# Kernel optimization log

Hardware: AMD Instinct MI355X
Metric: run time of the kernel (lower is better)

The kernel has to match this reference:

```python
import jax, jax.numpy as jnp
import numpy as np

N_NODES = 100000
N_EDGES = 1600000
D_FEAT = 64
EPS = 1e-07


def setup_inputs() -> dict:
    key = jax.random.key(0)
    k1, k2, k3 = jax.random.split(key, 3)
    x = jax.random.normal(k1, (N_NODES, D_FEAT), dtype=jnp.float32)
    beta = jnp.ones((1,), dtype=jnp.float32)
    edge_row = jnp.sort(jax.random.randint(k2, (N_EDGES,), 0, N_NODES, dtype=jnp.int64))
    edge_col = jax.random.randint(k3, (N_EDGES,), 0, N_NODES, dtype=jnp.int64)
    return {"x": x, "beta": beta, "edge_row": edge_row, "edge_col": edge_col}


def reference(x, beta, edge_row, edge_col):
    # Gather endpoint features: [E, d]
    A = x[edge_row]
    B = x[edge_col]
    # Cosine similarity per edge, scaled by beta: [E]
    inner = jnp.sum(A * B, axis=1)
    norms = jnp.linalg.norm(A, axis=1) * jnp.linalg.norm(B, axis=1)
    sim = beta[0] * (inner / (norms + EPS))
    # Sparse row-wise softmax (tf.sparse.softmax): stable segment softmax over edges grouped by row
    row_max = jax.ops.segment_max(sim, edge_row, num_segments=N_NODES)
    e = jnp.exp(sim - row_max[edge_row])
    row_sum = jax.ops.segment_sum(e, edge_row, num_segments=N_NODES)
    p = e / row_sum[edge_row]  # [E]
    # SPMM: out[i] = sum_{(i,j) in E} p_ij * x[j]
    out = jax.ops.segment_sum(p[:, None] * B, edge_row, num_segments=N_NODES)
    return out
```

## Files before the change

kernel.cpp:

```cpp
#include <hip/hip_runtime.h>
#include <math.h>

#define D_FEAT 64
typedef _Float16 v8h __attribute__((ext_vector_type(8)));
typedef _Float16 v4h __attribute__((ext_vector_type(4)));
typedef float v4f __attribute__((ext_vector_type(4)));

static __device__ __forceinline__ v8h u2h8(uint4 u){ v8h v; __builtin_memcpy(&v,&u,16); return v; }
static __device__ __forceinline__ v4h u2h4(uint2 u){ v4h v; __builtin_memcpy(&v,&u,8); return v; }
static __device__ __forceinline__ float f16lo(unsigned int m){
    unsigned short us = (unsigned short)(m & 0xffffu);
    _Float16 h; __builtin_memcpy(&h, &us, 2); return (float)h;
}

__global__ __launch_bounds__(256)
void agnn_prep1(const float* __restrict__ x, float* __restrict__ nf,
                uint2* __restrict__ xh, int n_nodes) {
    int t = blockIdx.x*blockDim.x + threadIdx.x;
    int node = t >> 4; if (node >= n_nodes) return;
    int l4 = t & 15;
    float4 v = ((const float4*)x)[node*16 + l4];
    float ss = v.x*v.x + v.y*v.y + v.z*v.z + v.w*v.w;
    #pragma unroll
    for (int off = 1; off < 16; off <<= 1) ss += __shfl_xor(ss, off, 64);
    float r = ss > 0.f ? rsqrtf(ss) : 0.f;
    if (l4 == 0) nf[node] = ss * r;
    auto h0 = __builtin_amdgcn_cvt_pkrtz(v.x*r, v.y*r);
    auto h1 = __builtin_amdgcn_cvt_pkrtz(v.z*r, v.w*r);
    uint2 u; __builtin_memcpy(&u.x, &h0, 4); __builtin_memcpy(&u.y, &h1, 4);
    xh[node*16 + l4] = u;
}

__global__ __launch_bounds__(256)
void agnn_prep2(const int* __restrict__ edge_row, const int* __restrict__ edge_col,
                const float* __restrict__ nf, int* __restrict__ row_ptr,
                unsigned int* __restrict__ md, int n_nodes, int n_edges) {
    int e = blockIdx.x*blockDim.x + threadIdx.x;
    if (e < 64) md[n_edges + e] = 0xFFFF0000u;
    if (e >= n_edges) return;
    int r1 = edge_row[e];
    int r0 = (e == 0) ? -1 : edge_row[e-1];
    for (int r = r0+1; r <= r1; ++r) row_ptr[r] = e;
    if (e == n_edges-1)
        for (int r = r1+1; r <= n_nodes; ++r) row_ptr[r] = n_edges;
    _Float16 h = (_Float16)nf[edge_col[e]];
    unsigned short us; __builtin_memcpy(&us, &h, 2);
    md[e] = ((unsigned int)(r1 & 15) << 16) | us;
}

#define XCP_PITCH 144
__global__ __launch_bounds__(128, 6)
void agnn_fused(const float* __restrict__ beta_p,
                const int* __restrict__ edge_col,
                const unsigned int* __restrict__ md,
                const int* __restrict__ row_ptr,
                const uint4* __restrict__ xh4,
                float* __restrict__ out, int n_nodes) {
    __shared__ char lds_raw[2 * 32 * XCP_PITCH];
    int wid = threadIdx.x >> 6, lane = threadIdx.x & 63;
    int q = lane >> 4, lo4 = lane & 15;
    char* XCP = lds_raw + wid * 32 * XCP_PITCH;

    int t0 = (blockIdx.x*2 + wid) * 16;
    if (t0 >= n_nodes) return;

    int qn = t0 + lo4; if (qn >= n_nodes) qn = n_nodes - 1;
    v8h b0 = u2h8(xh4[(size_t)qn*8 + q]);
    v8h b1 = u2h8(xh4[(size_t)qn*8 + 4 + q]);
    float beta  = beta_p[0];
    float shift = fabsf(beta);
    int te = t0 + 16; if (te > n_nodes) te = n_nodes;
    int es = row_ptr[t0];
    int L  = row_ptr[te] - es;

    v4f o0={0,0,0,0}, o1={0,0,0,0}, o2={0,0,0,0}, o3={0,0,0,0};
    float s = 0.f;
    unsigned int selp = (lo4 & 1) ? 0x07060302u : 0x05040100u;

    for (int base = 0; base < L; base += 32) {
        int i0 = base + lo4;
        int e0 = es + (i0 < L ? i0 : 0);
        int i1 = base + 16 + lo4;
        int e1 = es + (i1 < L ? i1 : 0);
        int c0 = edge_col[e0];
        int c1 = edge_col[e1];
        uint4 A00 = xh4[(size_t)c0*8 + q];
        uint4 A01 = xh4[(size_t)c0*8 + 4 + q];
        uint4 A10 = xh4[(size_t)c1*8 + q];
        uint4 A11 = xh4[(size_t)c1*8 + 4 + q];
        int mb = es + base + 4*q;
        unsigned int m00 = md[mb+0],  m01 = md[mb+1],  m02 = md[mb+2],  m03 = md[mb+3];
        unsigned int m10 = md[mb+16], m11 = md[mb+17], m12 = md[mb+18], m13 = md[mb+19];

        v4f z0 = {0,0,0,0};
        z0 = __builtin_amdgcn_mfma_f32_16x16x32_f16(u2h8(A00), b0, z0, 0,0,0);
        z0 = __builtin_amdgcn_mfma_f32_16x16x32_f16(u2h8(A01), b1, z0, 0,0,0);
        v4f z1 = {0,0,0,0};
        z1 = __builtin_amdgcn_mfma_f32_16x16x32_f16(u2h8(A10), b0, z1, 0,0,0);
        z1 = __builtin_amdgcn_mfma_f32_16x16x32_f16(u2h8(A11), b1, z1, 0,0,0);

        {
            unsigned int colA = lo4*4, colB = (16+lo4)*4;
            char* pA = XCP + (4*q)*XCP_PITCH;
            char* pB = XCP + (16+4*q)*XCP_PITCH;
            *(unsigned int*)(pA + 0*XCP_PITCH + colA) = A00.x;
            *(unsigned int*)(pA + 1*XCP_PITCH + colA) = A00.y;
            *(unsigned int*)(pA + 2*XCP_PITCH + colA) = A00.z;
            *(unsigned int*)(pA + 3*XCP_PITCH + colA) = A00.w;
            *(unsigned int*)(pB + 0*XCP_PITCH + colA) = A01.x;
            *(unsigned int*)(pB + 1*XCP_PITCH + colA) = A01.y;
            *(unsigned int*)(pB + 2*XCP_PITCH + colA) = A01.z;
            *(unsigned int*)(pB + 3*XCP_PITCH + colA) = A01.w;
            *(unsigned int*)(pA + 0*XCP_PITCH + colB) = A10.x;
            *(unsigned int*)(pA + 1*XCP_PITCH + colB) = A10.y;
            *(unsigned int*)(pA + 2*XCP_PITCH + colB) = A10.z;
            *(unsigned int*)(pA + 3*XCP_PITCH + colB) = A10.w;
            *(unsigned int*)(pB + 0*XCP_PITCH + colB) = A11.x;
            *(unsigned int*)(pB + 1*XCP_PITCH + colB) = A11.y;
            *(unsigned int*)(pB + 2*XCP_PITCH + colB) = A11.z;
            *(unsigned int*)(pB + 3*XCP_PITCH + colB) = A11.w;
        }

        int lim0 = L - base - 4*q;
        int lim1 = lim0 - 16;
        float w00 = (0 < lim0 && (m00>>16)==(unsigned)lo4) ? __expf(fmaf(beta, z0[0], -shift)) : 0.f;
        float w01 = (1 < lim0 && (m01>>16)==(unsigned)lo4) ? __expf(fmaf(beta, z0[1], -shift)) : 0.f;
        float w02 = (2 < lim0 && (m02>>16)==(unsigned)lo4) ? __expf(fmaf(beta, z0[2], -shift)) : 0.f;
        float w03 = (3 < lim0 && (m03>>16)==(unsigned)lo4) ? __expf(fmaf(beta, z0[3], -shift)) : 0.f;
        float w10 = (0 < lim1 && (m10>>16)==(unsigned)lo4) ? __expf(fmaf(beta, z1[0], -shift)) : 0.f;
        float w11 = (1 < lim1 && (m11>>16)==(unsigned)lo4) ? __expf(fmaf(beta, z1[1], -shift)) : 0.f;
        float w12 = (2 < lim1 && (m12>>16)==(unsigned)lo4) ? __expf(fmaf(beta, z1[2], -shift)) : 0.f;
        float w13 = (3 < lim1 && (m13>>16)==(unsigned)lo4) ? __expf(fmaf(beta, z1[3], -shift)) : 0.f;
        s += (w00+w01) + (w02+w03) + (w10+w11) + (w12+w13);

        v4h pa0, pa1;
        {
            auto a = __builtin_amdgcn_cvt_pkrtz(w00*f16lo(m00), w01*f16lo(m01));
            auto b = __builtin_amdgcn_cvt_pkrtz(w02*f16lo(m02), w03*f16lo(m03));
            pa0[0]=a[0]; pa0[1]=a[1]; pa0[2]=b[0]; pa0[3]=b[1];
            auto c = __builtin_amdgcn_cvt_pkrtz(w10*f16lo(m10), w11*f16lo(m11));
            auto d = __builtin_amdgcn_cvt_pkrtz(w12*f16lo(m12), w13*f16lo(m13));
            pa1[0]=c[0]; pa1[1]=c[1]; pa1[2]=d[0]; pa1[3]=d[1];
        }

        const char* rbase_p = XCP + (lo4>>1)*XCP_PITCH + 16*q;
        {
            const char* rp = rbase_p;
            uint4 d0 = *(const uint4*)rp;
            uint4 d1 = *(const uint4*)(rp + 64);
            uint2 bb0 = { __builtin_amdgcn_perm(d0.y, d0.x, selp), __builtin_amdgcn_perm(d0.w, d0.z, selp) };
            uint2 bb1 = { __builtin_amdgcn_perm(d1.y, d1.x, selp), __builtin_amdgcn_perm(d1.w, d1.z, selp) };
            o0 = __builtin_amdgcn_mfma_f32_16x16x16f16(pa0, u2h4(bb0), o0, 0,0,0);
            o0 = __builtin_amdgcn_mfma_f32_16x16x16f16(pa1, u2h4(bb1), o0, 0,0,0);
        }
        {
            const char* rp = rbase_p + 8*XCP_PITCH;
            uint4 d0 = *(const uint4*)rp;
            uint4 d1 = *(const uint4*)(rp + 64);
            uint2 bb0 = { __builtin_amdgcn_perm(d0.y, d0.x, selp), __builtin_amdgcn_perm(d0.w, d0.z, selp) };
            uint2 bb1 = { __builtin_amdgcn_perm(d1.y, d1.x, selp), __builtin_amdgcn_perm(d1.w, d1.z, selp) };
            o1 = __builtin_amdgcn_mfma_f32_16x16x16f16(pa0, u2h4(bb0), o1, 0,0,0);
            o1 = __builtin_amdgcn_mfma_f32_16x16x16f16(pa1, u2h4(bb1), o1, 0,0,0);
        }
        {
            const char* rp = rbase_p + 16*XCP_PITCH;
            uint4 d0 = *(const uint4*)rp;
            uint4 d1 = *(const uint4*)(rp + 64);
            uint2 bb0 = { __builtin_amdgcn_perm(d0.y, d0.x, selp), __builtin_amdgcn_perm(d0.w, d0.z, selp) };
            uint2 bb1 = { __builtin_amdgcn_perm(d1.y, d1.x, selp), __builtin_amdgcn_perm(d1.w, d1.z, selp) };
            o2 = __builtin_amdgcn_mfma_f32_16x16x16f16(pa0, u2h4(bb0), o2, 0,0,0);
            o2 = __builtin_amdgcn_mfma_f32_16x16x16f16(pa1, u2h4(bb1), o2, 0,0,0);
        }
        {
            const char* rp = rbase_p + 24*XCP_PITCH;
            uint4 d0 = *(const uint4*)rp;
            uint4 d1 = *(const uint4*)(rp + 64);
            uint2 bb0 = { __builtin_amdgcn_perm(d0.y, d0.x, selp), __builtin_amdgcn_perm(d0.w, d0.z, selp) };
            uint2 bb1 = { __builtin_amdgcn_perm(d1.y, d1.x, selp), __builtin_amdgcn_perm(d1.w, d1.z, selp) };
            o3 = __builtin_amdgcn_mfma_f32_16x16x16f16(pa0, u2h4(bb0), o3, 0,0,0);
            o3 = __builtin_amdgcn_mfma_f32_16x16x16f16(pa1, u2h4(bb1), o3, 0,0,0);
        }
    }

    s += __shfl_xor(s, 16, 64);
    s += __shfl_xor(s, 32, 64);

    #pragma unroll
    for (int r = 0; r < 4; ++r) {
        float sr = __shfl(s, 4*q + r, 64);
        float inv = sr > 0.f ? 1.f/sr : 0.f;
        int node = t0 + 4*q + r;
        if (node < n_nodes) {
            float* p = out + (size_t)node*64 + lo4;
            p[0]  = o0[r]*inv;
            p[16] = o1[r]*inv;
            p[32] = o2[r]*inv;
            p[48] = o3[r]*inv;
        }
    }
}

extern "C" void kernel_launch(void* const* d_in, const int* in_sizes, int n_in,
                              void* d_out, int out_size, void* d_ws, size_t ws_size,
                              hipStream_t stream) {
    const float* x        = (const float*)d_in[0];
    const float* beta     = (const float*)d_in[1];
    const int*   edge_row = (const int*)d_in[2];
    const int*   edge_col = (const int*)d_in[3];
    float* out = (float*)d_out;

    int n_nodes = in_sizes[0] / D_FEAT;
    int n_edges = in_sizes[2];

    char* ws = (char*)d_ws;
    float* nf = (float*)ws;
    size_t off0 = ((size_t)n_nodes*sizeof(float) + 255) & ~(size_t)255;
    int* row_ptr = (int*)(ws + off0);
    size_t off1 = off0 + (((size_t)(n_nodes+1)*sizeof(int) + 255) & ~(size_t)255);
    unsigned int* md = (unsigned int*)(ws + off1);
    size_t off2 = off1 + (((size_t)(n_edges+64)*sizeof(unsigned int) + 255) & ~(size_t)255);
    uint2* xh = (uint2*)(ws + off2);

    {
        long long threads = (long long)n_nodes * 16;
        int blocks = (int)((threads + 255) / 256);
        agnn_prep1<<<blocks, 256, 0, stream>>>(x, nf, xh, n_nodes);
    }
    {
        int blocks = (n_edges + 255) / 256;
        agnn_prep2<<<blocks, 256, 0, stream>>>(edge_row, edge_col, nf, row_ptr,
                                               md, n_nodes, n_edges);
    }
    {
        int tiles  = (n_nodes + 15) / 16;
        int blocks = (tiles + 1) / 2;
        agnn_fused<<<blocks, 128, 0, stream>>>(beta, edge_col, md, row_ptr,
                                               (const uint4*)xh, out, n_nodes);
    }
}
```

Before: 134.2 us.

## Software-pipeline gather loads in fused AGNN kernel and use 256-thread blocks

The fused kernel's edge loop now issues the next chunk's edge_col, feature and metadata loads before doing the MFMA, exp and LDS work on the current chunk. This register double-buffering is meant to hide the latency of the dependent global gathers. The block size also goes from 2 to 4 waves, and the occupancy hint (min 6 blocks) in launch_bounds is dropped. The extra registers held across the loop may lower occupancy.

```diff
diff --git a/kernel.cpp b/kernel.cpp
--- a/kernel.cpp
+++ b/kernel.cpp
@@ -49,19 +49,19 @@
 }
 
 #define XCP_PITCH 144
-__global__ __launch_bounds__(128, 6)
+__global__ __launch_bounds__(256)
 void agnn_fused(const float* __restrict__ beta_p,
                 const int* __restrict__ edge_col,
                 const unsigned int* __restrict__ md,
                 const int* __restrict__ row_ptr,
                 const uint4* __restrict__ xh4,
                 float* __restrict__ out, int n_nodes) {
-    __shared__ char lds_raw[2 * 32 * XCP_PITCH];
+    __shared__ char lds_raw[4 * 32 * XCP_PITCH];
     int wid = threadIdx.x >> 6, lane = threadIdx.x & 63;
     int q = lane >> 4, lo4 = lane & 15;
     char* XCP = lds_raw + wid * 32 * XCP_PITCH;
 
-    int t0 = (blockIdx.x*2 + wid) * 16;
+    int t0 = (blockIdx.x*4 + wid) * 16;
     if (t0 >= n_nodes) return;
 
     int qn = t0 + lo4; if (qn >= n_nodes) qn = n_nodes - 1;
@@ -77,10 +77,9 @@
     float s = 0.f;
     unsigned int selp = (lo4 & 1) ? 0x07060302u : 0x05040100u;
 
-    for (int base = 0; base < L; base += 32) {
-        int i0 = base + lo4;
+    if (L > 0) {
+        int i0 = lo4, i1 = 16 + lo4;
         int e0 = es + (i0 < L ? i0 : 0);
-        int i1 = base + 16 + lo4;
         int e1 = es + (i1 < L ? i1 : 0);
         int c0 = edge_col[e0];
         int c1 = edge_col[e1];
@@ -88,97 +87,123 @@
         uint4 A01 = xh4[(size_t)c0*8 + 4 + q];
         uint4 A10 = xh4[(size_t)c1*8 + q];
         uint4 A11 = xh4[(size_t)c1*8 + 4 + q];
-        int mb = es + base + 4*q;
+        int mb = es + 4*q;
         unsigned int m00 = md[mb+0],  m01 = md[mb+1],  m02 = md[mb+2],  m03 = md[mb+3];
         unsigned int m10 = md[mb+16], m11 = md[mb+17], m12 = md[mb+18], m13 = md[mb+19];
 
-        v4f z0 = {0,0,0,0};
-        z0 = __builtin_amdgcn_mfma_f32_16x16x32_f16(u2h8(A00), b0, z0, 0,0,0);
-        z0 = __builtin_amdgcn_mfma_f32_16x16x32_f16(u2h8(A01), b1, z0, 0,0,0);
-        v4f z1 = {0,0,0,0};
-        z1 = __builtin_amdgcn_mfma_f32_16x16x32_f16(u2h8(A10), b0, z1, 0,0,0);
-        z1 = __builtin_amdgcn_mfma_f32_16x16x32_f16(u2h8(A11), b1, z1, 0,0,0);
-
-        {
-            unsigned int colA = lo4*4, colB = (16+lo4)*4;
-            char* pA = XCP + (4*q)*XCP_PITCH;
-            char* pB = XCP + (16+4*q)*XCP_PITCH;
-            *(unsigned int*)(pA + 0*XCP_PITCH + colA) = A00.x;
-            *(unsigned int*)(pA + 1*XCP_PITCH + colA) = A00.y;
-            *(unsigned int*)(pA + 2*XCP_PITCH + colA) = A00.z;
-            *(unsigned int*)(pA + 3*XCP_PITCH + colA) = A00.w;
-            *(unsigned int*)(pB + 0*XCP_PITCH + colA) = A01.x;
-            *(unsigned int*)(pB + 1*XCP_PITCH + colA) = A01.y;
-            *(unsigned int*)(pB + 2*XCP_PITCH + colA) = A01.z;
-            *(unsigned int*)(pB + 3*XCP_PITCH + colA) = A01.w;
-            *(unsigned int*)(pA + 0*XCP_PITCH + colB) = A10.x;
-            *(unsigned int*)(pA + 1*XCP_PITCH + colB) = A10.y;
-            *(unsigned int*)(pA + 2*XCP_PITCH + colB) = A10.z;
-            *(unsigned int*)(pA + 3*XCP_PITCH + colB) = A10.w;
-            *(unsigned int*)(pB + 0*XCP_PITCH + colB) = A11.x;
-            *(unsigned int*)(pB + 1*XCP_PITCH + colB) = A11.y;
-            *(unsigned int*)(pB + 2*XCP_PITCH + colB) = A11.z;
-            *(unsigned int*)(pB + 3*XCP_PITCH + colB) = A11.w;
-        }
-
-        int lim0 = L - base - 4*q;
-        int lim1 = lim0 - 16;
-        float w00 = (0 < lim0 && (m00>>16)==(unsigned)lo4) ? __expf(fmaf(beta, z0[0], -shift)) : 0.f;
-        float w01 = (1 < lim0 && (m01>>16)==(unsigned)lo4) ? __expf(fmaf(beta, z0[1], -shift)) : 0.f;
-        float w02 = (2 < lim0 && (m02>>16)==(unsigned)lo4) ? __expf(fmaf(beta, z0[2], -shift)) : 0.f;
-        float w03 = (3 < lim0 && (m03>>16)==(unsigned)lo4) ? __expf(fmaf(beta, z0[3], -shift)) : 0.f;
-        float w10 = (0 < lim1 && (m10>>16)==(unsigned)lo4) ? __expf(fmaf(beta, z1[0], -shift)) : 0.f;
-        float w11 = (1 < lim1 && (m11>>16)==(unsigned)lo4) ? __expf(fmaf(beta, z1[1], -shift)) : 0.f;
-        float w12 = (2 < lim1 && (m12>>16)==(unsigned)lo4) ? __expf(fmaf(beta, z1[2], -shift)) : 0.f;
-        float w13 = (3 < lim1 && (m13>>16)==(unsigned)lo4) ? __expf(fmaf(beta, z1[3], -shift)) : 0.f;
-        s += (w00+w01) + (w02+w03) + (w10+w11) + (w12+w13);
-
-        v4h pa0, pa1;
-        {
-            auto a = __builtin_amdgcn_cvt_pkrtz(w00*f16lo(m00), w01*f16lo(m01));
-            auto b = __builtin_amdgcn_cvt_pkrtz(w02*f16lo(m02), w03*f16lo(m03));
-            pa0[0]=a[0]; pa0[1]=a[1]; pa0[2]=b[0]; pa0[3]=b[1];
-            auto c = __builtin_amdgcn_cvt_pkrtz(w10*f16lo(m10), w11*f16lo(m11));
-            auto d = __builtin_amdgcn_cvt_pkrtz(w12*f16lo(m12), w13*f16lo(m13));
-            pa1[0]=c[0]; pa1[1]=c[1]; pa1[2]=d[0]; pa1[3]=d[1];
-        }
-
-        const char* rbase_p = XCP + (lo4>>1)*XCP_PITCH + 16*q;
-        {
-            const char* rp = rbase_p;
-            uint4 d0 = *(const uint4*)rp;
-            uint4 d1 = *(const uint4*)(rp + 64);
-            uint2 bb0 = { __builtin_amdgcn_perm(d0.y, d0.x, selp), __builtin_amdgcn_perm(d0.w, d0.z, selp) };
-            uint2 bb1 = { __builtin_amdgcn_perm(d1.y, d1.x, selp), __builtin_amdgcn_perm(d1.w, d1.z, selp) };
-            o0 = __builtin_amdgcn_mfma_f32_16x16x16f16(pa0, u2h4(bb0), o0, 0,0,0);
-            o0 = __builtin_amdgcn_mfma_f32_16x16x16f16(pa1, u2h4(bb1), o0, 0,0,0);
-        }
-        {
-            const char* rp = rbase_p + 8*XCP_PITCH;
-            uint4 d0 = *(const uint4*)rp;
-            uint4 d1 = *(const uint4*)(rp + 64);
-            uint2 bb0 = { __builtin_amdgcn_perm(d0.y, d0.x, selp), __builtin_amdgcn_perm(d0.w, d0.z, selp) };
-            uint2 bb1 = { __builtin_amdgcn_perm(d1.y, d1.x, selp), __builtin_amdgcn_perm(d1.w, d1.z, selp) };
-            o1 = __builtin_amdgcn_mfma_f32_16x16x16f16(pa0, u2h4(bb0), o1, 0,0,0);
-            o1 = __builtin_amdgcn_mfma_f32_16x16x16f16(pa1, u2h4(bb1), o1, 0,0,0);
-        }
-        {
-            const char* rp = rbase_p + 16*XCP_PITCH;
-            uint4 d0 = *(const uint4*)rp;
-            uint4 d1 = *(const uint4*)(rp + 64);
-            uint2 bb0 = { __builtin_amdgcn_perm(d0.y, d0.x, selp), __builtin_amdgcn_perm(d0.w, d0.z, selp) };
-            uint2 bb1 = { __builtin_amdgcn_perm(d1.y, d1.x, selp), __builtin_amdgcn_perm(d1.w, d1.z, selp) };
-            o2 = __builtin_amdgcn_mfma_f32_16x16x16f16(pa0, u2h4(bb0), o2, 0,0,0);
-            o2 = __builtin_amdgcn_mfma_f32_16x16x16f16(pa1, u2h4(bb1), o2, 0,0,0);
-        }
-        {
-            const char* rp = rbase_p + 24*XCP_PITCH;
-            uint4 d0 = *(const uint4*)rp;
-            uint4 d1 = *(const uint4*)(rp + 64);
-            uint2 bb0 = { __builtin_amdgcn_perm(d0.y, d0.x, selp), __builtin_amdgcn_perm(d0.w, d0.z, selp) };
-            uint2 bb1 = { __builtin_amdgcn_perm(d1.y, d1.x, selp), __builtin_amdgcn_perm(d1.w, d1.z, selp) };
-            o3 = __builtin_amdgcn_mfma_f32_16x16x16f16(pa0, u2h4(bb0), o3, 0,0,0);
-            o3 = __builtin_amdgcn_mfma_f32_16x16x16f16(pa1, u2h4(bb1), o3, 0,0,0);
+        for (int base = 0; base < L; base += 32) {
+            bool more = (base + 32) < L;
+            uint4 B00, B01, B10, B11;
+            unsigned int n00, n01, n02, n03, n10, n11, n12, n13;
+            if (more) {
+                int j0 = base + 32 + lo4, j1 = base + 48 + lo4;
+                int f0 = es + (j0 < L ? j0 : 0);
+                int f1 = es + (j1 < L ? j1 : 0);
+                int d0 = edge_col[f0];
+                int d1 = edge_col[f1];
+                B00 = xh4[(size_t)d0*8 + q];
+                B01 = xh4[(size_t)d0*8 + 4 + q];
+                B10 = xh4[(size_t)d1*8 + q];
+                B11 = xh4[(size_t)d1*8 + 4 + q];
+                int nb = es + base + 32 + 4*q;
+                n00 = md[nb+0];  n01 = md[nb+1];  n02 = md[nb+2];  n03 = md[nb+3];
+                n10 = md[nb+16]; n11 = md[nb+17]; n12 = md[nb+18]; n13 = md[nb+19];
+            }
+
+            v4f z0 = {0,0,0,0};
+            z0 = __builtin_amdgcn_mfma_f32_16x16x32_f16(u2h8(A00), b0, z0, 0,0,0);
+            z0 = __builtin_amdgcn_mfma_f32_16x16x32_f16(u2h8(A01), b1, z0, 0,0,0);
+            v4f z1 = {0,0,0,0};
+            z1 = __builtin_amdgcn_mfma_f32_16x16x32_f16(u2h8(A10), b0, z1, 0,0,0);
+            z1 = __builtin_amdgcn_mfma_f32_16x16x32_f16(u2h8(A11), b1, z1, 0,0,0);
+
+            {
+                unsigned int colA = lo4*4, colB = (16+lo4)*4;
+                char* pA = XCP + (4*q)*XCP_PITCH;
+                char* pB = XCP + (16+4*q)*XCP_PITCH;
+                *(unsigned int*)(pA + 0*XCP_PITCH + colA) = A00.x;
+                *(unsigned int*)(pA + 1*XCP_PITCH + colA) = A00.y;
+                *(unsigned int*)(pA + 2*XCP_PITCH + colA) = A00.z;
+                *(unsigned int*)(pA + 3*XCP_PITCH + colA) = A00.w;
+                *(unsigned int*)(pB + 0*XCP_PITCH + colA) = A01.x;
+                *(unsigned int*)(pB + 1*XCP_PITCH + colA) = A01.y;
+                *(unsigned int*)(pB + 2*XCP_PITCH + colA) = A01.z;
+                *(unsigned int*)(pB + 3*XCP_PITCH + colA) = A01.w;
+                *(unsigned int*)(pA + 0*XCP_PITCH + colB) = A10.x;
+                *(unsigned int*)(pA + 1*XCP_PITCH + colB) = A10.y;
+                *(unsigned int*)(pA + 2*XCP_PITCH + colB) = A10.z;
+                *(unsigned int*)(pA + 3*XCP_PITCH + colB) = A10.w;
+                *(unsigned int*)(pB + 0*XCP_PITCH + colB) = A11.x;
+                *(unsigned int*)(pB + 1*XCP_PITCH + colB) = A11.y;
+                *(unsigned int*)(pB + 2*XCP_PITCH + colB) = A11.z;
+                *(unsigned int*)(pB + 3*XCP_PITCH + colB) = A11.w;
+            }
+
+            int lim0 = L - base - 4*q;
+            int lim1 = lim0 - 16;
+            float w00 = (0 < lim0 && (m00>>16)==(unsigned)lo4) ? __expf(fmaf(beta, z0[0], -shift)) : 0.f;
+            float w01 = (1 < lim0 && (m01>>16)==(unsigned)lo4) ? __expf(fmaf(beta, z0[1], -shift)) : 0.f;
+            float w02 = (2 < lim0 && (m02>>16)==(unsigned)lo4) ? __expf(fmaf(beta, z0[2], -shift)) : 0.f;
+            float w03 = (3 < lim0 && (m03>>16)==(unsigned)lo4) ? __expf(fmaf(beta, z0[3], -shift)) : 0.f;
+            float w10 = (0 < lim1 && (m10>>16)==(unsigned)lo4) ? __expf(fmaf(beta, z1[0], -shift)) : 0.f;
+            float w11 = (1 < lim1 && (m11>>16)==(unsigned)lo4) ? __expf(fmaf(beta, z1[1], -shift)) : 0.f;
+            float w12 = (2 < lim1 && (m12>>16)==(unsigned)lo4) ? __expf(fmaf(beta, z1[2], -shift)) : 0.f;
+            float w13 = (3 < lim1 && (m13>>16)==(unsigned)lo4) ? __expf(fmaf(beta, z1[3], -shift)) : 0.f;
+            s += (w00+w01) + (w02+w03) + (w10+w11) + (w12+w13);
+
+            v4h pa0, pa1;
+            {
+                auto a = __builtin_amdgcn_cvt_pkrtz(w00*f16lo(m00), w01*f16lo(m01));
+                auto b = __builtin_amdgcn_cvt_pkrtz(w02*f16lo(m02), w03*f16lo(m03));
+                pa0[0]=a[0]; pa0[1]=a[1]; pa0[2]=b[0]; pa0[3]=b[1];
+                auto c = __builtin_amdgcn_cvt_pkrtz(w10*f16lo(m10), w11*f16lo(m11));
+                auto d = __builtin_amdgcn_cvt_pkrtz(w12*f16lo(m12), w13*f16lo(m13));
+                pa1[0]=c[0]; pa1[1]=c[1]; pa1[2]=d[0]; pa1[3]=d[1];
+            }
+
+            const char* rbase_p = XCP + (lo4>>1)*XCP_PITCH + 16*q;
+            {
+                const char* rp = rbase_p;
+                uint4 d0 = *(const uint4*)rp;
+                uint4 d1 = *(const uint4*)(rp + 64);
+                uint2 bb0 = { __builtin_amdgcn_perm(d0.y, d0.x, selp), __builtin_amdgcn_perm(d0.w, d0.z, selp) };
+                uint2 bb1 = { __builtin_amdgcn_perm(d1.y, d1.x, selp), __builtin_amdgcn_perm(d1.w, d1.z, selp) };
+                o0 = __builtin_amdgcn_mfma_f32_16x16x16f16(pa0, u2h4(bb0), o0, 0,0,0);
+                o0 = __builtin_amdgcn_mfma_f32_16x16x16f16(pa1, u2h4(bb1), o0, 0,0,0);
+            }
+            {
+                const char* rp = rbase_p + 8*XCP_PITCH;
+                uint4 d0 = *(const uint4*)rp;
+                uint4 d1 = *(const uint4*)(rp + 64);
+                uint2 bb0 = { __builtin_amdgcn_perm(d0.y, d0.x, selp), __builtin_amdgcn_perm(d0.w, d0.z, selp) };
+                uint2 bb1 = { __builtin_amdgcn_perm(d1.y, d1.x, selp), __builtin_amdgcn_perm(d1.w, d1.z, selp) };
+                o1 = __builtin_amdgcn_mfma_f32_16x16x16f16(pa0, u2h4(bb0), o1, 0,0,0);
+                o1 = __builtin_amdgcn_mfma_f32_16x16x16f16(pa1, u2h4(bb1), o1, 0,0,0);
+            }
+            {
+                const char* rp = rbase_p + 16*XCP_PITCH;
+                uint4 d0 = *(const uint4*)rp;
+                uint4 d1 = *(const uint4*)(rp + 64);
+                uint2 bb0 = { __builtin_amdgcn_perm(d0.y, d0.x, selp), __builtin_amdgcn_perm(d0.w, d0.z, selp) };
+                uint2 bb1 = { __builtin_amdgcn_perm(d1.y, d1.x, selp), __builtin_amdgcn_perm(d1.w, d1.z, selp) };
+                o2 = __builtin_amdgcn_mfma_f32_16x16x16f16(pa0, u2h4(bb0), o2, 0,0,0);
+                o2 = __builtin_amdgcn_mfma_f32_16x16x16f16(pa1, u2h4(bb1), o2, 0,0,0);
+            }
+            {
+                const char* rp = rbase_p + 24*XCP_PITCH;
+                uint4 d0 = *(const uint4*)rp;
+                uint4 d1 = *(const uint4*)(rp + 64);
+                uint2 bb0 = { __builtin_amdgcn_perm(d0.y, d0.x, selp), __builtin_amdgcn_perm(d0.w, d0.z, selp) };
+                uint2 bb1 = { __builtin_amdgcn_perm(d1.y, d1.x, selp), __builtin_amdgcn_perm(d1.w, d1.z, selp) };
+                o3 = __builtin_amdgcn_mfma_f32_16x16x16f16(pa0, u2h4(bb0), o3, 0,0,0);
+                o3 = __builtin_amdgcn_mfma_f32_16x16x16f16(pa1, u2h4(bb1), o3, 0,0,0);
+            }
+
+            if (more) {
+                A00 = B00; A01 = B01; A10 = B10; A11 = B11;
+                m00 = n00; m01 = n01; m02 = n02; m03 = n03;
+                m10 = n10; m11 = n11; m12 = n12; m13 = n13;
+            }
         }
     }
 
@@ -233,8 +258,8 @@
     }
     {
         int tiles  = (n_nodes + 15) / 16;
-        int blocks = (tiles + 1) / 2;
-        agnn_fused<<<blocks, 128, 0, stream>>>(beta, edge_col, md, row_ptr,
+        int blocks = (tiles + 3) / 4;
+        agnn_fused<<<blocks, 256, 0, stream>>>(beta, edge_col, md, row_ptr,
                                                (const uint4*)xh, out, n_nodes);
     }
 }
```

New measurement: 138.1 us. 1.03x slower.

## Split each node tile's edge loop across two waves and combine via LDS

Applied to the files above, without the earlier changes.

Each 16-node tile is now processed by two waves, with the edge chunks interleaved between them. The second wave stores its partial output accumulators and softmax sums to LDS, and the first wave adds them in and writes the normalized result. This doubles the waves in flight and halves the serial edge loop per wave, at the cost of a block-wide barrier, LDS traffic for the combine, and a relaxed launch bound that may change register allocation.

```diff
diff --git a/kernel.cpp b/kernel.cpp
--- a/kernel.cpp
+++ b/kernel.cpp
@@ -49,35 +49,44 @@
 }
 
 #define XCP_PITCH 144
-__global__ __launch_bounds__(128, 6)
+#define WAVE_LDS_B (32 * XCP_PITCH)
+__global__ __launch_bounds__(256)
 void agnn_fused(const float* __restrict__ beta_p,
                 const int* __restrict__ edge_col,
                 const unsigned int* __restrict__ md,
                 const int* __restrict__ row_ptr,
                 const uint4* __restrict__ xh4,
                 float* __restrict__ out, int n_nodes) {
-    __shared__ char lds_raw[2 * 32 * XCP_PITCH];
+    __shared__ __align__(16) char lds_raw[4 * WAVE_LDS_B];
     int wid = threadIdx.x >> 6, lane = threadIdx.x & 63;
     int q = lane >> 4, lo4 = lane & 15;
-    char* XCP = lds_raw + wid * 32 * XCP_PITCH;
-
-    int t0 = (blockIdx.x*2 + wid) * 16;
-    if (t0 >= n_nodes) return;
-
-    int qn = t0 + lo4; if (qn >= n_nodes) qn = n_nodes - 1;
+    int sub = wid & 1;
+    char* XCP = lds_raw + wid * WAVE_LDS_B;
+
+    int tile = blockIdx.x*2 + (wid >> 1);
+    int t0 = tile * 16;
+    bool tile_ok = t0 < n_nodes;
+
+    int qn = t0 + lo4;
+    if (qn >= n_nodes) qn = n_nodes - 1;
+    if (qn < 0) qn = 0;
     v8h b0 = u2h8(xh4[(size_t)qn*8 + q]);
     v8h b1 = u2h8(xh4[(size_t)qn*8 + 4 + q]);
     float beta  = beta_p[0];
     float shift = fabsf(beta);
-    int te = t0 + 16; if (te > n_nodes) te = n_nodes;
-    int es = row_ptr[t0];
-    int L  = row_ptr[te] - es;
+
+    int es = 0, L = 0;
+    if (tile_ok) {
+        int te = t0 + 16; if (te > n_nodes) te = n_nodes;
+        es = row_ptr[t0];
+        L  = row_ptr[te] - es;
+    }
 
     v4f o0={0,0,0,0}, o1={0,0,0,0}, o2={0,0,0,0}, o3={0,0,0,0};
     float s = 0.f;
     unsigned int selp = (lo4 & 1) ? 0x07060302u : 0x05040100u;
 
-    for (int base = 0; base < L; base += 32) {
+    for (int base = sub*32; base < L; base += 64) {
         int i0 = base + lo4;
         int e0 = es + (i0 < L ? i0 : 0);
         int i1 = base + 16 + lo4;
@@ -182,20 +191,44 @@
         }
     }
 
-    s += __shfl_xor(s, 16, 64);
-    s += __shfl_xor(s, 32, 64);
-
-    #pragma unroll
-    for (int r = 0; r < 4; ++r) {
-        float sr = __shfl(s, 4*q + r, 64);
-        float inv = sr > 0.f ? 1.f/sr : 0.f;
-        int node = t0 + 4*q + r;
-        if (node < n_nodes) {
-            float* p = out + (size_t)node*64 + lo4;
-            p[0]  = o0[r]*inv;
-            p[16] = o1[r]*inv;
-            p[32] = o2[r]*inv;
-            p[48] = o3[r]*inv;
+    if (sub == 1) {
+        float* cb = (float*)(lds_raw + wid * WAVE_LDS_B);
+        #pragma unroll
+        for (int r = 0; r < 4; ++r) {
+            cb[(0*4+r)*64 + lane] = o0[r];
+            cb[(1*4+r)*64 + lane] = o1[r];
+            cb[(2*4+r)*64 + lane] = o2[r];
+            cb[(3*4+r)*64 + lane] = o3[r];
+        }
+        cb[16*64 + lane] = s;
+    }
+    __syncthreads();
+    if (sub == 0 && tile_ok) {
+        const float* cb = (const float*)(lds_raw + (wid + 1) * WAVE_LDS_B);
+        #pragma unroll
+        for (int r = 0; r < 4; ++r) {
+            o0[r] += cb[(0*4+r)*64 + lane];
+            o1[r] += cb[(1*4+r)*64 + lane];
+            o2[r] += cb[(2*4+r)*64 + lane];
+            o3[r] += cb[(3*4+r)*64 + lane];
+        }
+        s += cb[16*64 + lane];
+
+        s += __shfl_xor(s, 16, 64);
+        s += __shfl_xor(s, 32, 64);
+
+        #pragma unroll
+        for (int r = 0; r < 4; ++r) {
+            float sr = __shfl(s, 4*q + r, 64);
+            float inv = sr > 0.f ? 1.f/sr : 0.f;
+            int node = t0 + 4*q + r;
+            if (node < n_nodes) {
+                float* p = out + (size_t)node*64 + lo4;
+                p[0]  = o0[r]*inv;
+                p[16] = o1[r]*inv;
+                p[32] = o2[r]*inv;
+                p[48] = o3[r]*inv;
+            }
         }
     }
 }
@@ -234,7 +267,7 @@
     {
         int tiles  = (n_nodes + 15) / 16;
         int blocks = (tiles + 1) / 2;
-        agnn_fused<<<blocks, 128, 0, stream>>>(beta, edge_col, md, row_ptr,
+        agnn_fused<<<blocks, 256, 0, stream>>>(beta, edge_col, md, row_ptr,
                                                (const uint4*)xh, out, n_nodes);
     }
 }
```

Result: slower. 137.8 us (+2.7%).
